# Kernel optimization log

Hardware: AMD Instinct MI355X
Metric: run time of the kernel (lower is better)

## Reference

```python
import jax, jax.numpy as jnp
import numpy as np

DIM = 1024
DEPTH = 4
HEADS = 16
DIM_HEAD = 64
INNER = HEADS * DIM_HEAD  # 1024
FF_INNER = 4 * DIM
EPS = 1e-5


def _layer_norm(x, g, b):
    mu = jnp.mean(x, axis=-1, keepdims=True)
    var = jnp.mean(jnp.square(x - mu), axis=-1, keepdims=True)
    return (x - mu) * jax.lax.rsqrt(var + EPS) * g + b


def setup_inputs() -> dict:
    key = jax.random.key(0)
    ks = jax.random.split(key, 8)
    s = 0.02
    return {
        "x": jax.random.normal(ks[0], (2, 2048, DIM), dtype=jnp.float32),
        "mask": jnp.ones((2, 2048), dtype=bool),
        "ln1_g": jnp.ones((DEPTH, DIM), jnp.float32),
        "ln1_b": jnp.zeros((DEPTH, DIM), jnp.float32),
        "wqkv": jax.random.normal(ks[1], (DEPTH, DIM, 3 * INNER), jnp.float32) * s,
        "wo": jax.random.normal(ks[2], (DEPTH, INNER, DIM), jnp.float32) * s,
        "ln2_g": jnp.ones((DEPTH, DIM), jnp.float32),
        "ln2_b": jnp.zeros((DEPTH, DIM), jnp.float32),
        "w1": jax.random.normal(ks[3], (DEPTH, DIM, FF_INNER), jnp.float32) * s,
        "b1": jnp.zeros((DEPTH, FF_INNER), jnp.float32),
        "w2": jax.random.normal(ks[4], (DEPTH, FF_INNER, DIM), jnp.float32) * s,
        "b2": jnpp if False else jnp.zeros((DEPTH, DIM), jnp.float32),
    }


def _attention(x, mask, wqkv, wo):
    b, n, _ = x.shape
    qkv = x @ wqkv  # [b, n, 3*inner]
    q, k, v = jnp.split(qkv, 3, axis=-1)
    def heads(t):
        return t.reshape(b, n, HEADS, DIM_HEAD).transpose(0, 2, 1, 3)  # b h n d
    q, k, v = heads(q), heads(k), heads(v)
    scale = DIM_HEAD ** -0.5
    dots = jnp.einsum('bhid,bhjd->bhij', q, k) * scale
    neg = -jnp.finfo(dots.dtype).max
    dots = jnp.where(mask[:, None, None, :], dots, neg)
    attn = jax.nn.softmax(dots, axis=-1)
    out = jnp.einsum('bhij,bhjd->bhid', attn, v)
    out = out.transpose(0, 2, 1, 3).reshape(b, n, INNER)
    return out @ wo


def reference(x, mask, ln1_g, ln1_b, wqkv, wo, ln2_g, ln2_b, w1, b1, w2, b2):
    for l in range(DEPTH):
        x = _attention(_layer_norm(x, ln1_g[l], ln1_b[l]), mask, wqkv[l], wo[l]) + x
        h = _layer_norm(x, ln2_g[l], ln2_b[l])
        h = jax.nn.gelu(h @ w1[l] + b1[l], approximate=False) @ w2[l] + b2[l]
        x = h + x
    return x
```

## Files before the change

### kernel.cpp

```cpp
#include <hip/hip_runtime.h>

using u16 = unsigned short;
typedef __attribute__((ext_vector_type(8))) short short8;
typedef __attribute__((ext_vector_type(4))) short short4v;
typedef __attribute__((ext_vector_type(4))) float floatx4;

#define SEQ   2048
#define NROWS 4096
#define NDIM  1024
#define QKV_N 3072
#define FF_N  4096

__device__ __forceinline__ u16 f2bf(float f) {
  unsigned u = __builtin_bit_cast(unsigned, f);
  u += 0x7FFFu + ((u >> 16) & 1u);
  return (u16)(u >> 16);
}
__device__ __forceinline__ u16 f2bt(float f) {
  return (u16)(__builtin_bit_cast(unsigned, f) >> 16);
}
__device__ __forceinline__ float bf2f(u16 h) {
  unsigned u = ((unsigned)h) << 16;
  return __builtin_bit_cast(float, u);
}

__device__ __forceinline__ void gl_lds16(const void* g, void* l) {
  __builtin_amdgcn_global_load_lds(
      (const __attribute__((address_space(1))) unsigned int*)(uintptr_t)g,
      (__attribute__((address_space(3))) unsigned int*)(uintptr_t)l, 16, 0, 0);
}

__launch_bounds__(256)
__global__ void kconv_t(const float* __restrict__ in, u16* __restrict__ out,
                        int K, int N) {
  __shared__ float tile[64][65];
  int k0 = blockIdx.y * 64, n0 = blockIdx.x * 64;
  int t = threadIdx.x;
  int lrow = t >> 4;
  int lc4 = (t & 15) * 4;
#pragma unroll
  for (int r = 0; r < 4; r++) {
    int k = lrow + r * 16;
    float4 v = *(const float4*)&in[(size_t)(k0 + k) * N + n0 + lc4];
    tile[k][lc4 + 0] = v.x;
    tile[k][lc4 + 1] = v.y;
    tile[k][lc4 + 2] = v.z;
    tile[k][lc4 + 3] = v.w;
  }
  __syncthreads();
  int n = t >> 2;
  int kc = (t & 3) * 16;
  short8 o0, o1;
#pragma unroll
  for (int j = 0; j < 8; j++) o0[j] = (short)f2bf(tile[kc + j][n]);
#pragma unroll
  for (int j = 0; j < 8; j++) o1[j] = (short)f2bf(tile[kc + 8 + j][n]);
  *(short8*)&out[(size_t)(n0 + n) * K + k0 + kc] = o0;
  *(short8*)&out[(size_t)(n0 + n) * K + k0 + kc + 8] = o1;
}

__launch_bounds__(256)
__global__ void kln(const float* __restrict__ x, const float* __restrict__ g,
                    const float* __restrict__ b, u16* __restrict__ out) {
  int row = blockIdx.x;
  int t = threadIdx.x;
  const float4* xr = (const float4*)(x + (size_t)row * NDIM);
  float4 v = xr[t];
  float s = v.x + v.y + v.z + v.w;
  float ss = v.x * v.x + v.y * v.y + v.z * v.z + v.w * v.w;
#pragma unroll
  for (int m = 1; m < 64; m <<= 1) {
    s += __shfl_xor(s, m);
    ss += __shfl_xor(ss, m);
  }
  __shared__ float red[8];
  if ((t & 63) == 0) { red[t >> 6] = s; red[4 + (t >> 6)] = ss; }
  __syncthreads();
  s = red[0] + red[1] + red[2] + red[3];
  ss = red[4] + red[5] + red[6] + red[7];
  float mu = s * (1.0f / NDIM);
  float rs = rsqrtf(ss * (1.0f / NDIM) - mu * mu + 1e-5f);
  float4 gv = ((const float4*)g)[t];
  float4 bv = ((const float4*)b)[t];
  short4v ov;
  ov[0] = (short)f2bf((v.x - mu) * rs * gv.x + bv.x);
  ov[1] = (short)f2bf((v.y - mu) * rs * gv.y + bv.y);
  ov[2] = (short)f2bf((v.z - mu) * rs * gv.z + bv.z);
  ov[3] = (short)f2bf((v.w - mu) * rs * gv.w + bv.w);
  *(short4v*)&out[(size_t)row * NDIM + t * 4] = ov;
}

template <int EPI>
__launch_bounds__(512, 2)
__global__ void kgemm256(const u16* __restrict__ A, const u16* __restrict__ Bt,
                         int K, int N, const float* __restrict__ bias,
                         void* __restrict__ out, void* __restrict__ out2,
                         void* __restrict__ out3) {
  __shared__ __align__(16) char ldsA[2][32768];
  __shared__ __align__(16) char ldsB[2][32768];
  int nx = gridDim.x;
  int id = blockIdx.y * nx + blockIdx.x;
  int cpx = (nx * gridDim.y) >> 3;
  int sw = (id & 7) * cpx + (id >> 3);
  int m0 = (sw % nx) * 256;
  int n0 = (sw / nx) * 256;
  int t = threadIdx.x;
  int l = t & 63, w = t >> 6;
  int wmrow = (w >> 2) * 128;
  int wnrow = (w & 3) * 64;
  int lr = l & 15;
  int lg = l >> 4;
  int NT2 = K >> 6;

  int srcsw = ((l & 7) ^ (l >> 3)) * 8;
  auto stageA = [&](int tile, int u) {
    char* dst = ldsA[tile & 1] + u * 1024;
    gl_lds16(&A[(size_t)(m0 + u * 8 + (l >> 3)) * K + (tile << 6) + srcsw], dst);
  };
  auto stageB = [&](int tile, int u) {
    char* dst = ldsB[tile & 1] + u * 1024;
    gl_lds16(&Bt[(size_t)(n0 + u * 8 + (l >> 3)) * K + (tile << 6) + srcsw], dst);
  };
  auto slot = [&](int tile, int s) {
    if (tile >= NT2) return;
    int e0 = 2 * w, e1 = 2 * w + 1;
    if (s == 0) {
      stageA(tile, e0 < 8 ? e0 : e0 + 8);
      stageA(tile, e1 < 8 ? e1 : e1 + 8);
    } else if (s == 1) {
      stageB(tile, (e0 >> 2) * 8 + (e0 & 3));
      stageB(tile, (e1 >> 2) * 8 + (e1 & 3));
    } else if (s == 2) {
      stageB(tile, (e0 >> 2) * 8 + 4 + (e0 & 3));
      stageB(tile, (e1 >> 2) * 8 + 4 + (e1 & 3));
    } else {
      stageA(tile, e0 < 8 ? e0 + 8 : e0 + 16);
      stageA(tile, e1 < 8 ? e1 + 8 : e1 + 16);
    }
  };

  floatx4 acc[8][4];
#pragma unroll
  for (int m = 0; m < 8; m++)
#pragma unroll
    for (int n = 0; n < 4; n++) acc[m][n] = (floatx4){0.f, 0.f, 0.f, 0.f};

  short8 af[4][2], bf0[2][2], bf1[2][2];
  auto loadAg = [&](int buf, int mg) {
#pragma unroll
    for (int mf = 0; mf < 4; mf++)
#pragma unroll
      for (int kh = 0; kh < 2; kh++) {
        int row = wmrow + (mg * 4 + mf) * 16 + lr;
        int ch = (kh * 4 + lg) ^ (row & 7);
        af[mf][kh] = *(const short8*)(ldsA[buf] + row * 128 + ch * 16);
      }
  };
  auto loadBg = [&](int buf, short8 (&bb)[2][2], int ng) {
#pragma unroll
    for (int nf = 0; nf < 2; nf++)
#pragma unroll
      for (int kh = 0; kh < 2; kh++) {
        int row = wnrow + (ng * 2 + nf) * 16 + lr;
        int ch = (kh * 4 + lg) ^ (row & 7);
        bb[nf][kh] = *(const short8*)(ldsB[buf] + row * 128 + ch * 16);
      }
  };
  auto doQ = [&](int mg, short8 (&bb)[2][2], int ng) {
    __builtin_amdgcn_s_setprio(1);
#pragma unroll
    for (int mf = 0; mf < 4; mf++)
#pragma unroll
      for (int nf = 0; nf < 2; nf++)
#pragma unroll
        for (int kh = 0; kh < 2; kh++)
          acc[mg * 4 + mf][ng * 2 + nf] =
              __builtin_amdgcn_mfma_f32_16x16x32_bf16(
                  af[mf][kh], bb[nf][kh], acc[mg * 4 + mf][ng * 2 + nf], 0, 0, 0);
    __builtin_amdgcn_s_setprio(0);
  };
#define FENCE asm volatile("" ::: "memory")
#define BAR __builtin_amdgcn_s_barrier()

#pragma unroll
  for (int s = 0; s < 4; s++) slot(0, s);
#pragma unroll
  for (int s = 0; s < 4; s++) slot(1, s);
  asm volatile("s_waitcnt vmcnt(0)" ::: "memory");
  BAR;

  int NI = NT2 >> 1;
  for (int i = 0; i < NI; i++) {
    int t0 = 2 * i, t1 = 2 * i + 1;
    loadAg(0, 0); loadBg(0, bf0, 0); FENCE;
    if (i > 0) slot(t1, 3);
    BAR; doQ(0, bf0, 0); BAR;
    loadBg(0, bf1, 1); FENCE;
    slot(t0 + 2, 0);
    BAR; doQ(0, bf1, 1); BAR;
    loadAg(0, 1); FENCE;
    slot(t0 + 2, 1);
    BAR; doQ(1, bf0, 0); BAR;
    slot(t0 + 2, 2);
    if (t0 + 2 < NT2) asm volatile("s_waitcnt vmcnt(6)" ::: "memory");
    else              asm volatile("s_waitcnt vmcnt(0)" ::: "memory");
    BAR; doQ(1, bf1, 1); BAR;
    loadAg(1, 0); loadBg(1, bf0, 0); FENCE;
    slot(t0 + 2, 3);
    BAR; doQ(0, bf0, 0); BAR;
    loadBg(1, bf1, 1); FENCE;
    slot(t1 + 2, 0);
    BAR; doQ(0, bf1, 1); BAR;
    loadAg(1, 1); FENCE;
    slot(t1 + 2, 1);
    BAR; doQ(1, bf0, 0); BAR;
    slot(t1 + 2, 2);
    if (t1 + 2 < NT2) asm volatile("s_waitcnt vmcnt(6)" ::: "memory");
    BAR; doQ(1, bf1, 1); BAR;
  }
#undef FENCE
#undef BAR

  int lq = lg * 4;
#pragma unroll
  for (int m = 0; m < 8; m++)
#pragma unroll
    for (int n = 0; n < 4; n++) {
      int row0 = m0 + wmrow + m * 16 + lq;
      int col = n0 + wnrow + n * 16 + lr;
      if (EPI == 4) {
        int bb = row0 >> 11, s = row0 & 2047;
        if (col < 2048) {
          int h = (col & 1023) >> 6, d = col & 63;
          u16* dst = (col < 1024) ? (u16*)out : (u16*)out2;
          size_t base = ((size_t)(bb * 16 + h) * SEQ + s) * 64 + d;
#pragma unroll
          for (int i2 = 0; i2 < 4; i2++)
            dst[base + (size_t)i2 * 64] = f2bf(acc[m][n][i2]);
        } else {
          int h = (col - 2048) >> 6, d = col & 63;
          short4v pv;
#pragma unroll
          for (int i2 = 0; i2 < 4; i2++) pv[i2] = (short)f2bf(acc[m][n][i2]);
          *(short4v*)&((u16*)out3)[((size_t)(bb * 16 + h) * 64 + d) * SEQ + s] = pv;
        }
      } else {
#pragma unroll
        for (int i2 = 0; i2 < 4; i2++) {
          float v = acc[m][n][i2] + bias[col];
          v = 0.5f * v * (1.0f + erff(v * 0.70710678118f));
          ((u16*)out)[(size_t)(row0 + i2) * N + col] = f2bf(v);
        }
      }
    }
}

#define BM 128
#define BN 128
#define BK 32

template <int EPI>
__launch_bounds__(256, 3)
__global__ void kgemm(const u16* __restrict__ A, const u16* __restrict__ Bt,
                      int K, int N, const float* __restrict__ bias,
                      const float* __restrict__ res, void* __restrict__ out) {
  __shared__ __align__(16) u16 As[3][BM * BK];
  __shared__ __align__(16) u16 Bs[3][BN * BK];
  int nx = gridDim.x;
  int id = blockIdx.y * nx + blockIdx.x;
  int cpx = (nx * gridDim.y) >> 3;
  int sw = (id & 7) * cpx + (id >> 3);
  int m0 = (sw % nx) * BM;
  int n0 = (sw / nx) * BN;
  int t = threadIdx.x;
  int l = t & 63, w = t >> 6;
  int wm = (w >> 1) * 64, wn = (w & 1) * 64;
  int lr = l & 15;

  int c16 = (l >> 4) * 16;
  int offA[4], offB[4];
#pragma unroll
  for (int m = 0; m < 4; m++) {
    int lin = (wm + m * 16 + lr) * 64 + c16;
    offA[m] = lin ^ (((lin >> 7) & 7) << 4);
  }
#pragma unroll
  for (int n = 0; n < 4; n++) {
    int lin = (wn + n * 16 + lr) * 64 + c16;
    offB[n] = lin ^ (((lin >> 7) & 7) << 4);
  }

  auto stage = [&](int tt, int bf) {
    int kk = tt << 5;
#pragma unroll
    for (int p = 0; p < 2; p++) {
      int u0 = p * 256 + w * 64;
      int u = u0 + l;
      int lin = (u * 16) ^ (((u >> 3) & 7) << 4);
      int row = lin >> 6;
      int col = (lin & 63) >> 1;
      gl_lds16(&A[(size_t)(m0 + row) * K + kk + col], (char*)As[bf] + u0 * 16);
      gl_lds16(&Bt[(size_t)(n0 + row) * K + kk + col], (char*)Bs[bf] + u0 * 16);
    }
  };

  floatx4 acc[4][4];
#pragma unroll
  for (int m = 0; m < 4; m++)
#pragma unroll
    for (int n = 0; n < 4; n++) acc[m][n] = (floatx4){0.f, 0.f, 0.f, 0.f};

  int NT = K >> 5;
  stage(0, 0);
  stage(1, 1);
  int ra = 0, rb = 1, rc = 2;

  for (int tt = 0; tt < NT; ++tt) {
    if (tt + 2 < NT) {
      stage(tt + 2, rc);
      asm volatile("s_waitcnt vmcnt(8)" ::: "memory");
    } else if (tt + 1 < NT) {
      asm volatile("s_waitcnt vmcnt(4)" ::: "memory");
    } else {
      asm volatile("s_waitcnt vmcnt(0)" ::: "memory");
    }
    __builtin_amdgcn_s_barrier();
    const char* Ab = (const char*)As[ra];
    const char* Bb = (const char*)Bs[ra];
    short8 af[4], bfr[4];
#pragma unroll
    for (int m = 0; m < 4; m++) af[m] = *(const short8*)(Ab + offA[m]);
#pragma unroll
    for (int n = 0; n < 4; n++) bfr[n] = *(const short8*)(Bb + offB[n]);
    __builtin_amdgcn_s_setprio(1);
#pragma unroll
    for (int m = 0; m < 4; m++)
#pragma unroll
      for (int n = 0; n < 4; n++)
        acc[m][n] = __builtin_amdgcn_mfma_f32_16x16x32_bf16(af[m], bfr[n],
                                                            acc[m][n], 0, 0, 0);
    __builtin_amdgcn_s_setprio(0);
    __builtin_amdgcn_s_barrier();
    int tmp = ra; ra = rb; rb = rc; rc = tmp;
  }

  int lq = (l >> 4) * 4;
#pragma unroll
  for (int m = 0; m < 4; m++)
#pragma unroll
    for (int n = 0; n < 4; n++)
#pragma unroll
      for (int i = 0; i < 4; i++) {
        int row = m0 + wm + m * 16 + lq + i;
        int col = n0 + wn + n * 16 + lr;
        float v = acc[m][n][i];
        if (EPI == 2) {
          v += res[(size_t)row * N + col];
          ((float*)out)[(size_t)row * N + col] = v;
        } else {
          v += bias[col] + res[(size_t)row * N + col];
          ((float*)out)[(size_t)row * N + col] = v;
        }
      }
}

#define KSTR 72
__launch_bounds__(512, 8)
__global__ void kflash(const u16* __restrict__ Qb, const u16* __restrict__ Kb,
                       const u16* __restrict__ Vb, u16* __restrict__ ao) {
  __shared__ __align__(16) u16 Ks[64 * 64];
  __shared__ __align__(16) u16 Vt[64 * 64];
  __shared__ __align__(16) u16 Ps[8][16 * KSTR];
  int t = threadIdx.x, l = t & 63, w = t >> 6;
  int bid = blockIdx.x;
  int xcd = bid & 7, sslot = bid >> 3;
  int bh = xcd + 8 * (sslot >> 4);
  int qc = sslot & 15;
  int b = bh >> 4, h = bh & 15;
  int q0 = qc * 128 + w * 16;
  int lr = l & 15, g = l >> 4, lk = g * 8;
  const u16* qbase = Qb + (size_t)(b * 16 + h) * SEQ * 64;
  const u16* kbase = Kb + (size_t)(b * 16 + h) * SEQ * 64;
  const u16* vbase = Vb + (size_t)(b * 16 + h) * 64 * SEQ;

  const float QSC = 0.125f * 1.44269504f;
  short8 qf[2];
#pragma unroll
  for (int k2 = 0; k2 < 2; k2++) {
    short8 v = *(const short8*)(qbase + (size_t)(q0 + lr) * 64 + k2 * 32 + lk);
#pragma unroll
    for (int j = 0; j < 8; j++) v[j] = (short)f2bf(bf2f((u16)v[j]) * QSC);
    qf[k2] = v;
  }

  short8 onesb;
#pragma unroll
  for (int j = 0; j < 8; j++) onesb[j] = (lr == 0) ? (short)0x3F80 : (short)0;

  floatx4 o[4], ol;
  float mrow[4];
  ol = (floatx4){0.f, 0.f, 0.f, 0.f};
#pragma unroll
  for (int n = 0; n < 4; n++) o[n] = (floatx4){0.f, 0.f, 0.f, 0.f};
#pragma unroll
  for (int i = 0; i < 4; i++) mrow[i] = -1e30f;

  for (int kv = 0; kv < SEQ; kv += 64) {
    __syncthreads();
    {
      int u0 = w * 64;
      int r = (u0 + l) >> 3;
      int cs = ((l & 7) ^ (r & 7)) * 8;
      gl_lds16(kbase + (size_t)(kv + r) * 64 + cs, &Ks[(size_t)u0 * 8]);
      gl_lds16(vbase + (size_t)r * SEQ + kv + cs, &Vt[(size_t)u0 * 8]);
    }
    __syncthreads();

    floatx4 s[4];
#pragma unroll
    for (int n = 0; n < 4; n++) s[n] = (floatx4){0.f, 0.f, 0.f, 0.f};
    __builtin_amdgcn_s_setprio(1);
#pragma unroll
    for (int n = 0; n < 4; n++)
#pragma unroll
      for (int k2 = 0; k2 < 2; k2++) {
        int row = n * 16 + lr;
        int byte = (row * 128 + (k2 * 32 + lk) * 2) ^ ((row & 7) << 4);
        short8 kb = *(const short8*)((const char*)Ks + byte);
        s[n] = __builtin_amdgcn_mfma_f32_16x16x32_bf16(qf[k2], kb, s[n], 0, 0, 0);
      }
    __builtin_amdgcn_s_setprio(0);

    float pmax[4];
    bool need = false;
#pragma unroll
    for (int i = 0; i < 4; i++) {
      float mx = fmaxf(fmaxf(s[0][i], s[1][i]), fmaxf(s[2][i], s[3][i]));
      pmax[i] = mx;
      need |= (mx > mrow[i] + 11.0f);
    }
    if (__any(need)) {
#pragma unroll
      for (int i = 0; i < 4; i++) {
        float mx = pmax[i];
#pragma unroll
        for (int d = 1; d < 16; d <<= 1) mx = fmaxf(mx, __shfl_xor(mx, d));
        float nm = fmaxf(mrow[i], mx);
        float corr = __builtin_amdgcn_exp2f(mrow[i] - nm);
        mrow[i] = nm;
#pragma unroll
        for (int n = 0; n < 4; n++) o[n][i] *= corr;
        ol[i] *= corr;
      }
    }
#pragma unroll
    for (int i = 0; i < 4; i++) {
      int prow = (g * 4 + i) * KSTR;
#pragma unroll
      for (int n = 0; n < 4; n++)
        Ps[w][prow + n * 16 + lr] = f2bt(__builtin_amdgcn_exp2f(s[n][i] - mrow[i]));
    }

    short8 pa[2];
#pragma unroll
    for (int k2 = 0; k2 < 2; k2++)
      pa[k2] = *(const short8*)&Ps[w][lr * KSTR + k2 * 32 + lk];
    __builtin_amdgcn_s_setprio(1);
#pragma unroll
    for (int n = 0; n < 4; n++)
#pragma unroll
      for (int k2 = 0; k2 < 2; k2++) {
        int d = n * 16 + lr;
        int byte = (d * 128 + (k2 * 32 + lk) * 2) ^ ((d & 7) << 4);
        short8 vb = *(const short8*)((const char*)Vt + byte);
        o[n] = __builtin_amdgcn_mfma_f32_16x16x32_bf16(pa[k2], vb, o[n], 0, 0, 0);
      }
#pragma unroll
    for (int k2 = 0; k2 < 2; k2++)
      ol = __builtin_amdgcn_mfma_f32_16x16x32_bf16(pa[k2], onesb, ol, 0, 0, 0);
    __builtin_amdgcn_s_setprio(0);
  }

#pragma unroll
  for (int i = 0; i < 4; i++) {
    float lsum = __shfl(ol[i], l & 48);
    float inv = 1.0f / lsum;
    int grow = b * SEQ + q0 + g * 4 + i;
#pragma unroll
    for (int n = 0; n < 4; n++)
      ao[(size_t)grow * NDIM + h * 64 + n * 16 + lr] = f2bt(o[n][i] * inv);
  }
}

extern "C" void kernel_launch(void* const* d_in, const int* in_sizes, int n_in,
                              void* d_out, int out_size, void* d_ws,
                              size_t ws_size, hipStream_t stream) {
  const float* x = (const float*)d_in[0];
  const float* ln1_g = (const float*)d_in[2];
  const float* ln1_b = (const float*)d_in[3];
  const float* wqkv = (const float*)d_in[4];
  const float* wo = (const float*)d_in[5];
  const float* ln2_g = (const float*)d_in[6];
  const float* ln2_b = (const float*)d_in[7];
  const float* w1 = (const float*)d_in[8];
  const float* b1 = (const float*)d_in[9];
  const float* w2 = (const float*)d_in[10];
  const float* b2 = (const float*)d_in[11];
  float* xout = (float*)d_out;

  char* ws = (char*)d_ws;
  size_t off = 0;
  auto alloc = [&](size_t bytes) {
    void* p = ws + off;
    off += (bytes + 255) & ~(size_t)255;
    return p;
  };
  u16* wqkv_t = (u16*)alloc((size_t)QKV_N * NDIM * 2);
  u16* wo_t = (u16*)alloc((size_t)NDIM * NDIM * 2);
  u16* w1_t = (u16*)alloc((size_t)FF_N * NDIM * 2);
  u16* w2_t = (u16*)alloc((size_t)NDIM * FF_N * 2);
  u16* actA = (u16*)alloc((size_t)NROWS * NDIM * 2);
  u16* actB = (u16*)alloc((size_t)NROWS * NDIM * 2);
  u16* big = (u16*)alloc((size_t)NROWS * FF_N * 2);
  u16* Qb = (u16*)alloc((size_t)NROWS * NDIM * 2);
  u16* Kbuf = (u16*)alloc((size_t)NROWS * NDIM * 2);
  u16* Vbuf = (u16*)alloc((size_t)NROWS * NDIM * 2);

  hipMemcpyAsync(xout, x, (size_t)NROWS * NDIM * 4, hipMemcpyDeviceToDevice,
                 stream);

  for (int lyr = 0; lyr < 4; lyr++) {
    kconv_t<<<dim3(QKV_N / 64, NDIM / 64), 256, 0, stream>>>(
        wqkv + (size_t)lyr * NDIM * QKV_N, wqkv_t, NDIM, QKV_N);
    kconv_t<<<dim3(NDIM / 64, NDIM / 64), 256, 0, stream>>>(
        wo + (size_t)lyr * NDIM * NDIM, wo_t, NDIM, NDIM);
    kconv_t<<<dim3(FF_N / 64, NDIM / 64), 256, 0, stream>>>(
        w1 + (size_t)lyr * NDIM * FF_N, w1_t, NDIM, FF_N);
    kconv_t<<<dim3(NDIM / 64, FF_N / 64), 256, 0, stream>>>(
        w2 + (size_t)lyr * FF_N * NDIM, w2_t, FF_N, NDIM);

    kln<<<NROWS, 256, 0, stream>>>(xout, ln1_g + lyr * NDIM,
                                   ln1_b + lyr * NDIM, actA);
    kgemm256<4><<<dim3(NROWS / 256, QKV_N / 256), 512, 0, stream>>>(
        actA, wqkv_t, NDIM, QKV_N, nullptr, Qb, Kbuf, Vbuf);
    kflash<<<dim3(512), 512, 0, stream>>>(Qb, Kbuf, Vbuf, actB);
    kgemm<2><<<dim3(NROWS / BM, NDIM / BN), 256, 0, stream>>>(
        actB, wo_t, NDIM, NDIM, nullptr, xout, xout);
    kln<<<NROWS, 256, 0, stream>>>(xout, ln2_g + lyr * NDIM,
                                   ln2_b + lyr * NDIM, actA);
    kgemm256<1><<<dim3(NROWS / 256, FF_N / 256), 512, 0, stream>>>(
        actA, w1_t, NDIM, FF_N, b1 + (size_t)lyr * FF_N, big, nullptr, nullptr);
    kgemm<3><<<dim3(NROWS / BM, NDIM / BN), 256, 0, stream>>>(
        big, w2_t, FF_N, NDIM, b2 + (size_t)lyr * NDIM, xout, xout);
  }
}
```

Baseline: 1.035 ms.

## Merge weight conversions into one launch and shrink flash attention blocks

The four per-layer weight transpose/convert kernels are merged into a single launch that picks which matrix to process from the block index, cutting three launches per layer. The flash attention kernel moves from 512-thread blocks over 128 query rows to 256-thread blocks over 64 query rows, doubling the grid to 1024 blocks. Each thread now issues two K/V load chunks per tile. Smaller blocks improve load balance and occupancy granularity, but each K/V tile is now reused by half as many queries, which doubles K/V traffic into LDS.

```diff
diff --git a/kernel.cpp b/kernel.cpp
--- a/kernel.cpp
+++ b/kernel.cpp
@@ -31,10 +31,30 @@
 }
 
 __launch_bounds__(256)
-__global__ void kconv_t(const float* __restrict__ in, u16* __restrict__ out,
-                        int K, int N) {
+__global__ void kconv4(const float* __restrict__ in_qkv,
+                       const float* __restrict__ in_wo,
+                       const float* __restrict__ in_w1,
+                       const float* __restrict__ in_w2,
+                       u16* __restrict__ o_qkv, u16* __restrict__ o_wo,
+                       u16* __restrict__ o_w1, u16* __restrict__ o_w2) {
+  int bid = blockIdx.x;
+  const float* in;
+  u16* out;
+  int K, N, tx, ty;
+  if (bid < 768) {
+    in = in_qkv; out = o_qkv; K = 1024; N = 3072; tx = bid % 48; ty = bid / 48;
+  } else if (bid < 1024) {
+    int r = bid - 768;
+    in = in_wo; out = o_wo; K = 1024; N = 1024; tx = r % 16; ty = r / 16;
+  } else if (bid < 2048) {
+    int r = bid - 1024;
+    in = in_w1; out = o_w1; K = 1024; N = 4096; tx = r % 64; ty = r / 64;
+  } else {
+    int r = bid - 2048;
+    in = in_w2; out = o_w2; K = 4096; N = 1024; tx = r % 16; ty = r / 16;
+  }
   __shared__ float tile[64][65];
-  int k0 = blockIdx.y * 64, n0 = blockIdx.x * 64;
+  int k0 = ty * 64, n0 = tx * 64;
   int t = threadIdx.x;
   int lrow = t >> 4;
   int lc4 = (t & 15) * 4;
@@ -365,19 +385,19 @@
 }
 
 #define KSTR 72
-__launch_bounds__(512, 8)
+__launch_bounds__(256, 4)
 __global__ void kflash(const u16* __restrict__ Qb, const u16* __restrict__ Kb,
                        const u16* __restrict__ Vb, u16* __restrict__ ao) {
   __shared__ __align__(16) u16 Ks[64 * 64];
   __shared__ __align__(16) u16 Vt[64 * 64];
-  __shared__ __align__(16) u16 Ps[8][16 * KSTR];
+  __shared__ __align__(16) u16 Ps[4][16 * KSTR];
   int t = threadIdx.x, l = t & 63, w = t >> 6;
   int bid = blockIdx.x;
   int xcd = bid & 7, sslot = bid >> 3;
-  int bh = xcd + 8 * (sslot >> 4);
-  int qc = sslot & 15;
+  int bh = xcd + 8 * (sslot >> 5);
+  int qc = sslot & 31;
   int b = bh >> 4, h = bh & 15;
-  int q0 = qc * 128 + w * 16;
+  int q0 = qc * 64 + w * 16;
   int lr = l & 15, g = l >> 4, lk = g * 8;
   const u16* qbase = Qb + (size_t)(b * 16 + h) * SEQ * 64;
   const u16* kbase = Kb + (size_t)(b * 16 + h) * SEQ * 64;
@@ -407,8 +427,9 @@
 
   for (int kv = 0; kv < SEQ; kv += 64) {
     __syncthreads();
-    {
-      int u0 = w * 64;
+#pragma unroll
+    for (int p = 0; p < 2; p++) {
+      int u0 = p * 256 + w * 64;
       int r = (u0 + l) >> 3;
       int cs = ((l & 7) ^ (r & 7)) * 8;
       gl_lds16(kbase + (size_t)(kv + r) * 64 + cs, &Ks[(size_t)u0 * 8]);
@@ -530,20 +551,16 @@
                  stream);
 
   for (int lyr = 0; lyr < 4; lyr++) {
-    kconv_t<<<dim3(QKV_N / 64, NDIM / 64), 256, 0, stream>>>(
-        wqkv + (size_t)lyr * NDIM * QKV_N, wqkv_t, NDIM, QKV_N);
-    kconv_t<<<dim3(NDIM / 64, NDIM / 64), 256, 0, stream>>>(
-        wo + (size_t)lyr * NDIM * NDIM, wo_t, NDIM, NDIM);
-    kconv_t<<<dim3(FF_N / 64, NDIM / 64), 256, 0, stream>>>(
-        w1 + (size_t)lyr * NDIM * FF_N, w1_t, NDIM, FF_N);
-    kconv_t<<<dim3(NDIM / 64, FF_N / 64), 256, 0, stream>>>(
-        w2 + (size_t)lyr * FF_N * NDIM, w2_t, FF_N, NDIM);
+    kconv4<<<dim3(3072), 256, 0, stream>>>(
+        wqkv + (size_t)lyr * NDIM * QKV_N, wo + (size_t)lyr * NDIM * NDIM,
+        w1 + (size_t)lyr * NDIM * FF_N, w2 + (size_t)lyr * FF_N * NDIM,
+        wqkv_t, wo_t, w1_t, w2_t);
 
     kln<<<NROWS, 256, 0, stream>>>(xout, ln1_g + lyr * NDIM,
                                    ln1_b + lyr * NDIM, actA);
     kgemm256<4><<<dim3(NROWS / 256, QKV_N / 256), 512, 0, stream>>>(
         actA, wqkv_t, NDIM, QKV_N, nullptr, Qb, Kbuf, Vbuf);
-    kflash<<<dim3(512), 512, 0, stream>>>(Qb, Kbuf, Vbuf, actB);
+    kflash<<<dim3(1024), 256, 0, stream>>>(Qb, Kbuf, Vbuf, actB);
     kgemm<2><<<dim3(NROWS / BM, NDIM / BN), 256, 0, stream>>>(
         actB, wo_t, NDIM, NDIM, nullptr, xout, xout);
     kln<<<NROWS, 256, 0, stream>>>(xout, ln2_g + lyr * NDIM,
```

New measurement: 957.6 us. 1.08x faster.
